# Kernel optimization log

Measured on AMD Instinct MI355X. Metric: run time of the kernel, lower is better.

## Reference

```python
import jax, jax.numpy as jnp
import numpy as np
import math

B, S, E, H, FF = 8, 1024, 1024, 16, 4096
HD = E // H
N_DOM = 1024          # boolean-domain size used in the custom scale
LN_EPS = 1e-5


def _layernorm(x, g, b, eps=LN_EPS):
    mu = jnp.mean(x, axis=-1, keepdims=True)
    var = jnp.var(x, axis=-1, keepdims=True)
    return (x - mu) * jax.lax.rsqrt(var + eps) * g + b


def setup_inputs() -> dict:
    key = jax.random.key(0)
    ks = jax.random.split(key, 8)
    s_e = 1.0 / math.sqrt(E)
    s_f = 1.0 / math.sqrt(FF)
    return {
        "x": jax.random.normal(ks[0], (B, S, E), jnp.float32),
        "in_proj_w": jax.random.normal(ks[1], (3 * E, E), jnp.float32) * s_e,
        "out_proj_w": jax.random.normal(ks[2], (E, E), jnp.float32) * s_e,
        "ln1_g": jnp.ones((E,), jnp.float32),
        "ln1_b": jnp.zeros((E,), jnp.float32),
        "ln2_g": jnp.ones((E,), jnp.float32),
        "ln2_b": jnp.zeros((E,), jnp.float32),
        "w1": jax.random.normal(ks[3], (FF, E), jnp.float32) * s_e,
        "b1": jax.random.normal(ks[4], (FF,), jnp.float32) * 0.01,
        "w2": jax.random.normal(ks[5], (E, FF), jnp.float32) * s_f,
        "b2": jax.random.normal(ks[6], (E,), jnp.float32) * 0.01,
    }


def reference(x, in_proj_w, out_proj_w, ln1_g, ln1_b, ln2_g, ln2_b, w1, b1, w2, b2):
    # --- custom multi-head attention (bias=False, dropout=0) ---
    qkv = jnp.einsum("bse,fe->bsf", x, in_proj_w)              # [B,S,3E]
    q, k, v = jnp.split(qkv, 3, axis=-1)
    q = q.reshape(B, S, H, HD)
    k = k.reshape(B, S, H, HD)
    v = v.reshape(B, S, H, HD)
    # nonstandard scale: sqrt(1/head_dim) * 2 * log(N)
    scale = math.sqrt(1.0 / HD) * 2.0 * math.log(N_DOM)
    scores = jnp.einsum("bqhd,bkhd->bhqk", q * scale, k)       # [B,H,S,S]
    attn = jax.nn.softmax(scores, axis=-1)
    ctx = jnp.einsum("bhqk,bkhd->bqhd", attn, v).reshape(B, S, E)
    attn_out = jnp.einsum("bse,fe->bsf", ctx, out_proj_w)      # [B,S,E]
    # --- residual + norm + FFN + residual + norm ---
    h = _layernorm(x + attn_out, ln1_g, ln1_b)
    ff = jnp.einsum("bsf,ef->bse", jax.nn.relu(jnp.einsum("bse,fe->bsf", h, w1) + b1), w2) + b2
    return _layernorm(h + ff, ln2_g, ln2_b)
```

## Files before the change

### kernel.cpp

```cpp
#include <hip/hip_runtime.h>
#include <cstdint>
#include <cmath>


typedef _Float16 f16;
typedef _Float16 f16x8 __attribute__((ext_vector_type(8)));
typedef _Float16 f16x4 __attribute__((ext_vector_type(4)));
typedef __bf16   bf16;
typedef __bf16   bf16x8 __attribute__((ext_vector_type(8)));
typedef __bf16   bf16x4 __attribute__((ext_vector_type(4)));
typedef float    f32x4  __attribute__((ext_vector_type(4)));

#define B_SZ  8
#define S_SZ  1024
#define E_SZ  1024
#define H_SZ  16
#define HD_SZ 64
#define FF_SZ 4096
#define MTOK  (B_SZ * S_SZ)

__device__ __forceinline__ void async_ld16(const void* g, void* l) {
  __builtin_amdgcn_global_load_lds(
      (const __attribute__((address_space(1))) void*)(uintptr_t)g,
      (__attribute__((address_space(3))) void*)(uint32_t)(uintptr_t)l,
      16, 0, 0);
}

__global__ void cast_kernel(const float* __restrict__ in, f16* __restrict__ out, int n4) {
  int i = blockIdx.x * blockDim.x + threadIdx.x;
  if (i < n4) {
    float4 f = ((const float4*)in)[i];
    f16x4 o = {(f16)f.x, (f16)f.y, (f16)f.z, (f16)f.w};
    ((f16x4*)out)[i] = o;
  }
}

template <bool OUT_F16, bool RELU>
__global__ void gemm_bt(const f16* __restrict__ A, const f16* __restrict__ Bm,
                        const float* __restrict__ bias, void* __restrict__ Cp,
                        int M, int N, int K, int bf16_from_bn) {
  __shared__ f16 As[128 * 64];
  __shared__ f16 Bs[128 * 64];

  const int tid  = threadIdx.x;
  const int wave = tid >> 6;
  const int lane = tid & 63;
  const int quad = lane >> 4;
  const int l16  = lane & 15;
  const int c7   = l16 & 7;
  const int wr   = wave >> 1;
  const int wc   = wave & 1;
  const int bm   = blockIdx.y;
  const int bn   = blockIdx.x;

  f32x4 acc[4][4];
#pragma unroll
  for (int i = 0; i < 4; i++)
#pragma unroll
    for (int j = 0; j < 4; j++) acc[i][j] = (f32x4){0.f, 0.f, 0.f, 0.f};

  const int rii  = wave * 8 + (lane >> 3);
  const int soct = (lane & 7) ^ (rii & 7);
  const f16* gA = A + ((size_t)bm * 128 + rii) * (size_t)K + soct * 8;
  const f16* gB = Bm + ((size_t)bn * 128 + rii) * (size_t)K + soct * 8;

  for (int k0 = 0; k0 < K; k0 += 64) {
    __syncthreads();
#pragma unroll
    for (int i = 0; i < 4; i++)
      async_ld16(gA + (size_t)i * 32 * K + k0, &As[(i * 32 + wave * 8) * 64]);
#pragma unroll
    for (int i = 0; i < 4; i++)
      async_ld16(gB + (size_t)i * 32 * K + k0, &Bs[(i * 32 + wave * 8) * 64]);
    __syncthreads();

#pragma unroll
    for (int kd2 = 0; kd2 < 2; kd2++) {
      f16x8 af[4], bfv[4];
#pragma unroll
      for (int mi = 0; mi < 4; mi++)
        af[mi] = *(const f16x8*)&As[(wr * 64 + mi * 16 + l16) * 64 + (((kd2 * 4 + quad) ^ c7) << 3)];
#pragma unroll
      for (int ni = 0; ni < 4; ni++)
        bfv[ni] = *(const f16x8*)&Bs[(wc * 64 + ni * 16 + l16) * 64 + (((kd2 * 4 + quad) ^ c7) << 3)];
#pragma unroll
      for (int mi = 0; mi < 4; mi++)
#pragma unroll
        for (int ni = 0; ni < 4; ni++)
          acc[mi][ni] = __builtin_amdgcn_mfma_f32_16x16x32_f16(af[mi], bfv[ni], acc[mi][ni], 0, 0, 0);
    }
  }

  const int rowBase = bm * 128 + wr * 64;
  const int colBase = bn * 128 + wc * 64;
  const bool store_bf16 = OUT_F16 && (bn >= bf16_from_bn);
#pragma unroll
  for (int ni = 0; ni < 4; ni++) {
    const int col = colBase + ni * 16 + l16;
    const float bv = (bias != nullptr) ? bias[col] : 0.f;
#pragma unroll
    for (int mi = 0; mi < 4; mi++) {
#pragma unroll
      for (int r = 0; r < 4; r++) {
        const int row = rowBase + mi * 16 + quad * 4 + r;
        float v = acc[mi][ni][r] + bv;
        if (RELU) v = fmaxf(v, 0.f);
        if (OUT_F16) {
          if (store_bf16)
            ((bf16*)Cp)[(size_t)row * N + col] = (bf16)v;
          else
            ((f16*)Cp)[(size_t)row * N + col] = (f16)v;
        } else {
          ((float*)Cp)[(size_t)row * N + col] = v;
        }
      }
    }
  }
}

__global__ __launch_bounds__(256, 3)
void attn_kernel(const f16* __restrict__ qkv, f16* __restrict__ ctx,
                 float scale2, float c2) {
  __shared__ __align__(16) char pool[49664];
  f16*  Qs = (f16*)pool;
  bf16* Ps = (bf16*)pool;
  bf16* Vt = (bf16*)(pool + 16384);
  f16*  Ks = (f16*)(pool + 33280);

  const int tid  = threadIdx.x;
  const int wave = tid >> 6;
  const int lane = tid & 63;
  const int quad = lane >> 4;
  const int l16  = lane & 15;
  const int c7   = l16 & 7;

  const int flat = blockIdx.x;
  const int bh   = flat & 127;
  const int qt   = flat >> 7;
  const int b    = bh >> 4;
  const int h    = bh & 15;

  const int rs = 3 * E_SZ;
  const size_t tokbase = (size_t)b * S_SZ;

  const int su  = lane >> 3;
  const int soc = (lane & 7) ^ su;

  {
    const f16* gq = qkv + (tokbase + qt * 128 + wave * 8 + su) * (size_t)rs + h * HD_SZ + soc * 8;
#pragma unroll
    for (int i = 0; i < 4; i++)
      async_ld16(gq + (size_t)i * 32 * rs, pool + (i * 32 + wave * 8) * 128);
  }
  __syncthreads();

  f16x8 aq[2][2];
#pragma unroll
  for (int mi = 0; mi < 2; mi++)
#pragma unroll
    for (int kd = 0; kd < 2; kd++) {
      const int row = wave * 32 + mi * 16 + l16;
      aq[mi][kd] = *(const f16x8*)&Qs[row * 64 + (((kd * 4 + quad) ^ c7) << 3)];
    }

  float Lpart[2] = {0.f, 0.f};
  f32x4 oacc[2][4];
#pragma unroll
  for (int mi = 0; mi < 2; mi++)
#pragma unroll
    for (int ni = 0; ni < 4; ni++) oacc[mi][ni] = (f32x4){0.f, 0.f, 0.f, 0.f};

  const int vc  = (tid & 7) * 8;
  const int vk0 = (tid >> 3) * 4;

  for (int t = 0; t < S_SZ / 128; t++) {
    __syncthreads();
    {
      const f16* gk = qkv + (tokbase + t * 128 + wave * 8 + su) * (size_t)rs + E_SZ + h * HD_SZ + soc * 8;
#pragma unroll
      for (int i = 0; i < 4; i++)
        async_ld16(gk + (size_t)i * 32 * rs, pool + 33280 + (i * 32 + wave * 8) * 128);
    }
    {
      const bf16* gv = (const bf16*)qkv + (tokbase + t * 128 + vk0) * (size_t)rs + 2 * E_SZ + h * HD_SZ + vc;
      bf16x8 v0 = *(const bf16x8*)(gv);
      bf16x8 v1 = *(const bf16x8*)(gv + rs);
      bf16x8 v2 = *(const bf16x8*)(gv + 2 * rs);
      bf16x8 v3 = *(const bf16x8*)(gv + 3 * rs);
#pragma unroll
      for (int e = 0; e < 8; e++) {
        bf16x4 pk = {v0[e], v1[e], v2[e], v3[e]};
        *(bf16x4*)&Vt[(vc + e) * 132 + vk0] = pk;
      }
    }
    __syncthreads();

    f32x4 sacc[2][8];
#pragma unroll
    for (int mi = 0; mi < 2; mi++)
#pragma unroll
      for (int nt = 0; nt < 8; nt++) sacc[mi][nt] = (f32x4){0.f, 0.f, 0.f, 0.f};
#pragma unroll
    for (int nt = 0; nt < 8; nt++) {
      const int krow = nt * 16 + l16;
#pragma unroll
      for (int kd = 0; kd < 2; kd++) {
        f16x8 bk = *(const f16x8*)&Ks[krow * 64 + (((kd * 4 + quad) ^ c7) << 3)];
#pragma unroll
        for (int mi = 0; mi < 2; mi++)
          sacc[mi][nt] = __builtin_amdgcn_mfma_f32_16x16x32_f16(bk, aq[mi][kd], sacc[mi][nt], 0, 0, 0);
      }
    }

#pragma unroll
    for (int mi = 0; mi < 2; mi++) {
#pragma unroll
      for (int nt = 0; nt < 8; nt++) {
#pragma unroll
        for (int r = 0; r < 4; r++) {
          float p = exp2f(fmaf(sacc[mi][nt][r], scale2, -c2));
          sacc[mi][nt][r] = p;
          Lpart[mi] += p;
        }
      }
    }

#pragma unroll
    for (int hf = 0; hf < 2; hf++) {
#pragma unroll
      for (int mi = 0; mi < 2; mi++) {
        const int prow = wave * 32 + mi * 16 + l16;
#pragma unroll
        for (int ntl = 0; ntl < 4; ntl++) {
          const f32x4 s4 = sacc[mi][hf * 4 + ntl];
          bf16x4 pk = {(bf16)s4[0], (bf16)s4[1], (bf16)s4[2], (bf16)s4[3]};
          const int oct = (2 * ntl + (quad >> 1)) ^ c7;
          *(bf16x4*)&Ps[prow * 64 + oct * 8 + (quad & 1) * 4] = pk;
        }
      }
#pragma unroll
      for (int kt = 0; kt < 2; kt++) {
        bf16x8 ap[2];
#pragma unroll
        for (int mi = 0; mi < 2; mi++) {
          const int prow = wave * 32 + mi * 16 + l16;
          ap[mi] = *(const bf16x8*)&Ps[prow * 64 + (((kt * 4 + quad) ^ c7) << 3)];
        }
#pragma unroll
        for (int ni = 0; ni < 4; ni++) {
          const int d = ni * 16 + l16;
          bf16x4 blo = *(const bf16x4*)&Vt[d * 132 + hf * 64 + kt * 32 + quad * 8];
          bf16x4 bhi = *(const bf16x4*)&Vt[d * 132 + hf * 64 + kt * 32 + quad * 8 + 4];
          bf16x8 bv = __builtin_shufflevector(blo, bhi, 0, 1, 2, 3, 4, 5, 6, 7);
#pragma unroll
          for (int mi = 0; mi < 2; mi++)
            oacc[mi][ni] = __builtin_amdgcn_mfma_f32_16x16x32_bf16(ap[mi], bv, oacc[mi][ni], 0, 0, 0);
        }
      }
    }
  }

#pragma unroll
  for (int mi = 0; mi < 2; mi++) {
    float Lfull = Lpart[mi];
    Lfull += __shfl_xor(Lfull, 16, 64);
    Lfull += __shfl_xor(Lfull, 32, 64);
#pragma unroll
    for (int r = 0; r < 4; r++) {
      const float Lr  = __shfl(Lfull, quad * 4 + r, 64);
      const float inv = 1.f / Lr;
      const int s = qt * 128 + wave * 32 + mi * 16 + quad * 4 + r;
#pragma unroll
      for (int ni = 0; ni < 4; ni++)
        ctx[(tokbase + s) * (size_t)E_SZ + h * HD_SZ + ni * 16 + l16] = (f16)(oacc[mi][ni][r] * inv);
    }
  }
}

__global__ void ln_kernel(const float* __restrict__ a, const float* __restrict__ res,
                          const float* __restrict__ g, const float* __restrict__ bta,
                          float* __restrict__ out32, f16* __restrict__ out16) {
  const int row  = blockIdx.x;
  const int tid  = threadIdx.x;
  const int wave = tid >> 6;
  const int lane = tid & 63;
  const size_t base = (size_t)row * 1024;
  const int c = tid * 4;

  float4 va = *(const float4*)&a[base + c];
  float4 vr = *(const float4*)&res[base + c];
  float v0 = va.x + vr.x, v1 = va.y + vr.y, v2 = va.z + vr.z, v3 = va.w + vr.w;

  __shared__ float r1[4], r2[4];
  float s = v0 + v1 + v2 + v3;
#pragma unroll
  for (int off = 32; off; off >>= 1) s += __shfl_xor(s, off, 64);
  if (lane == 0) r1[wave] = s;
  __syncthreads();
  const float mu = (r1[0] + r1[1] + r1[2] + r1[3]) * (1.f / 1024.f);

  float d0 = v0 - mu, d1 = v1 - mu, d2 = v2 - mu, d3 = v3 - mu;
  float ss = d0 * d0 + d1 * d1 + d2 * d2 + d3 * d3;
#pragma unroll
  for (int off = 32; off; off >>= 1) ss += __shfl_xor(ss, off, 64);
  if (lane == 0) r2[wave] = ss;
  __syncthreads();
  const float var = (r2[0] + r2[1] + r2[2] + r2[3]) * (1.f / 1024.f);
  const float rsq = rsqrtf(var + 1e-5f);

  float4 gg = *(const float4*)&g[c];
  float4 bb = *(const float4*)&bta[c];
  float o0 = d0 * rsq * gg.x + bb.x;
  float o1 = d1 * rsq * gg.y + bb.y;
  float o2 = d2 * rsq * gg.z + bb.z;
  float o3 = d3 * rsq * gg.w + bb.w;
  float4 o = {o0, o1, o2, o3};
  *(float4*)&out32[base + c] = o;
  if (out16 != nullptr) {
    f16x4 ob = {(f16)o0, (f16)o1, (f16)o2, (f16)o3};
    *(f16x4*)&out16[base + c] = ob;
  }
}

extern "C" void kernel_launch(void* const* d_in, const int* in_sizes, int n_in,
                              void* d_out, int out_size, void* d_ws, size_t ws_size,
                              hipStream_t stream) {
  const float* x    = (const float*)d_in[0];
  const float* wqkv = (const float*)d_in[1];
  const float* wo   = (const float*)d_in[2];
  const float* ln1g = (const float*)d_in[3];
  const float* ln1b = (const float*)d_in[4];
  const float* ln2g = (const float*)d_in[5];
  const float* ln2b = (const float*)d_in[6];
  const float* w1   = (const float*)d_in[7];
  const float* b1   = (const float*)d_in[8];
  const float* w2   = (const float*)d_in[9];
  const float* b2   = (const float*)d_in[10];
  float* out = (float*)d_out;

  char* ws = (char*)d_ws;
  f16* w_inb  = (f16*)(ws + 0);
  f16* w_outb = (f16*)(ws + 6291456);
  f16* w1b    = (f16*)(ws + 8388608);
  f16* w2b    = (f16*)(ws + 16777216);
  f16* xb     = (f16*)(ws + 25165824);
  f16* qkv    = (f16*)(ws + 41943040);
  f16* ctx    = (f16*)(ws + 92274688);
  f16* ff1    = (f16*)(ws + 41943040);
  float* tmp  = (float*)(ws + 109051904);
  float* hbuf = (float*)(ws + 142606336);
  f16* hb     = xb;

  const int NOBF = 1 << 30;

  cast_kernel<<<3072, 256, 0, stream>>>(wqkv, w_inb, 3 * E_SZ * E_SZ / 4);
  cast_kernel<<<1024, 256, 0, stream>>>(wo, w_outb, E_SZ * E_SZ / 4);
  cast_kernel<<<4096, 256, 0, stream>>>(w1, w1b, FF_SZ * E_SZ / 4);
  cast_kernel<<<4096, 256, 0, stream>>>(w2, w2b, E_SZ * FF_SZ / 4);
  cast_kernel<<<8192, 256, 0, stream>>>(x, xb, MTOK * E_SZ / 4);

  gemm_bt<true, false><<<dim3(3 * E_SZ / 128, MTOK / 128), 256, 0, stream>>>(
      xb, w_inb, nullptr, qkv, MTOK, 3 * E_SZ, E_SZ, 16);

  attn_kernel<<<1024, 256, 0, stream>>>(qkv, ctx, 2.5f, 60.0f);

  gemm_bt<false, false><<<dim3(E_SZ / 128, MTOK / 128), 256, 0, stream>>>(
      ctx, w_outb, nullptr, tmp, MTOK, E_SZ, E_SZ, NOBF);

  ln_kernel<<<MTOK, 256, 0, stream>>>(tmp, x, ln1g, ln1b, hbuf, hb);

  gemm_bt<true, true><<<dim3(FF_SZ / 128, MTOK / 128), 256, 0, stream>>>(
      hb, w1b, b1, ff1, MTOK, FF_SZ, E_SZ, NOBF);

  gemm_bt<false, false><<<dim3(E_SZ / 128, MTOK / 128), 256, 0, stream>>>(
      ff1, w2b, b2, tmp, MTOK, E_SZ, FF_SZ, NOBF);

  ln_kernel<<<MTOK, 256, 0, stream>>>(tmp, hbuf, ln2g, ln2b, out, nullptr);

  (void)in_sizes; (void)n_in; (void)out_size; (void)ws_size;
}
```

Baseline: 525.6 us.

## Use 32x32 MFMA in GEMMs, fuse residual adds, f16 intermediates, fold softmax scale

Switches the GEMM inner loop from 16x16x32 to 32x32x16 MFMA tiles. Residual additions move into the GEMM epilogues, and the intermediates become f16 instead of fp32, which removes an fp32 hidden buffer and shrinks LN traffic. The attention kernel pre-scales Q in f16 and starts the score accumulators at the softmax offset, dropping an FMA per score. The trade-off is lower precision: the residual stream is kept in f16, and the second residual uses the f16 LN1 output rather than fp32.

```diff
diff --git a/kernel.cpp b/kernel.cpp
--- a/kernel.cpp
+++ b/kernel.cpp
@@ -10,6 +10,7 @@
 typedef __bf16   bf16x8 __attribute__((ext_vector_type(8)));
 typedef __bf16   bf16x4 __attribute__((ext_vector_type(4)));
 typedef float    f32x4  __attribute__((ext_vector_type(4)));
+typedef float    f32x16 __attribute__((ext_vector_type(16)));
 
 #define B_SZ  8
 #define S_SZ  1024
@@ -35,12 +36,103 @@
   }
 }
 
-template <bool OUT_F16, bool RELU>
+template <bool RELU>
 __global__ void gemm_bt(const f16* __restrict__ A, const f16* __restrict__ Bm,
-                        const float* __restrict__ bias, void* __restrict__ Cp,
+                        const float* __restrict__ bias,
+                        const float* __restrict__ res32,
+                        const f16* __restrict__ res16,
+                        void* __restrict__ Cp,
                         int M, int N, int K, int bf16_from_bn) {
   __shared__ f16 As[128 * 64];
   __shared__ f16 Bs[128 * 64];
+
+  const int tid  = threadIdx.x;
+  const int wave = tid >> 6;
+  const int lane = tid & 63;
+  const int l32  = lane & 31;
+  const int hi   = lane >> 5;
+  const int wr   = wave >> 1;
+  const int wc   = wave & 1;
+  const int bm   = blockIdx.y;
+  const int bn   = blockIdx.x;
+
+  f32x16 acc[2][2];
+#pragma unroll
+  for (int i = 0; i < 2; i++)
+#pragma unroll
+    for (int j = 0; j < 2; j++)
+#pragma unroll
+      for (int e = 0; e < 16; e++) acc[i][j][e] = 0.f;
+
+  const int rii  = wave * 8 + (lane >> 3);
+  const int soct = (lane & 7) ^ (rii & 7);
+  const f16* gA = A + ((size_t)bm * 128 + rii) * (size_t)K + soct * 8;
+  const f16* gB = Bm + ((size_t)bn * 128 + rii) * (size_t)K + soct * 8;
+
+  for (int k0 = 0; k0 < K; k0 += 64) {
+    __syncthreads();
+#pragma unroll
+    for (int i = 0; i < 4; i++)
+      async_ld16(gA + (size_t)i * 32 * K + k0, &As[(i * 32 + wave * 8) * 64]);
+#pragma unroll
+    for (int i = 0; i < 4; i++)
+      async_ld16(gB + (size_t)i * 32 * K + k0, &Bs[(i * 32 + wave * 8) * 64]);
+    __syncthreads();
+
+#pragma unroll
+    for (int ph = 0; ph < 4; ph++) {
+      f16x8 af[2], bfv[2];
+#pragma unroll
+      for (int mi = 0; mi < 2; mi++) {
+        const int row = wr * 64 + mi * 32 + l32;
+        af[mi] = *(const f16x8*)&As[row * 64 + (((ph * 2 + hi) ^ (row & 7)) << 3)];
+      }
+#pragma unroll
+      for (int ni = 0; ni < 2; ni++) {
+        const int row = wc * 64 + ni * 32 + l32;
+        bfv[ni] = *(const f16x8*)&Bs[row * 64 + (((ph * 2 + hi) ^ (row & 7)) << 3)];
+      }
+#pragma unroll
+      for (int mi = 0; mi < 2; mi++)
+#pragma unroll
+        for (int ni = 0; ni < 2; ni++)
+          acc[mi][ni] = __builtin_amdgcn_mfma_f32_32x32x16_f16(af[mi], bfv[ni], acc[mi][ni], 0, 0, 0);
+    }
+  }
+
+  const int rowBase = bm * 128 + wr * 64;
+  const int colBase = bn * 128 + wc * 64;
+  const bool store_bf16 = (bn >= bf16_from_bn);
+#pragma unroll
+  for (int ni = 0; ni < 2; ni++) {
+    const int col = colBase + ni * 32 + l32;
+    const float bv = (bias != nullptr) ? bias[col] : 0.f;
+#pragma unroll
+    for (int mi = 0; mi < 2; mi++) {
+#pragma unroll
+      for (int reg = 0; reg < 16; reg++) {
+        const int row = rowBase + mi * 32 + (reg & 3) + 8 * (reg >> 2) + 4 * hi;
+        const size_t idx = (size_t)row * N + col;
+        float v = acc[mi][ni][reg] + bv;
+        if (res32 != nullptr) v += res32[idx];
+        else if (res16 != nullptr) v += (float)res16[idx];
+        if (RELU) v = fmaxf(v, 0.f);
+        if (store_bf16)
+          ((bf16*)Cp)[idx] = (bf16)v;
+        else
+          ((f16*)Cp)[idx] = (f16)v;
+      }
+    }
+  }
+}
+
+__global__ __launch_bounds__(256, 3)
+void attn_kernel(const f16* __restrict__ qkv, f16* __restrict__ ctx) {
+  __shared__ __align__(16) char pool[49664];
+  f16*  Qs = (f16*)pool;
+  bf16* Ps = (bf16*)pool;
+  bf16* Vt = (bf16*)(pool + 16384);
+  f16*  Ks = (f16*)(pool + 33280);
 
   const int tid  = threadIdx.x;
   const int wave = tid >> 6;
@@ -48,91 +140,6 @@
   const int quad = lane >> 4;
   const int l16  = lane & 15;
   const int c7   = l16 & 7;
-  const int wr   = wave >> 1;
-  const int wc   = wave & 1;
-  const int bm   = blockIdx.y;
-  const int bn   = blockIdx.x;
-
-  f32x4 acc[4][4];
-#pragma unroll
-  for (int i = 0; i < 4; i++)
-#pragma unroll
-    for (int j = 0; j < 4; j++) acc[i][j] = (f32x4){0.f, 0.f, 0.f, 0.f};
-
-  const int rii  = wave * 8 + (lane >> 3);
-  const int soct = (lane & 7) ^ (rii & 7);
-  const f16* gA = A + ((size_t)bm * 128 + rii) * (size_t)K + soct * 8;
-  const f16* gB = Bm + ((size_t)bn * 128 + rii) * (size_t)K + soct * 8;
-
-  for (int k0 = 0; k0 < K; k0 += 64) {
-    __syncthreads();
-#pragma unroll
-    for (int i = 0; i < 4; i++)
-      async_ld16(gA + (size_t)i * 32 * K + k0, &As[(i * 32 + wave * 8) * 64]);
-#pragma unroll
-    for (int i = 0; i < 4; i++)
-      async_ld16(gB + (size_t)i * 32 * K + k0, &Bs[(i * 32 + wave * 8) * 64]);
-    __syncthreads();
-
-#pragma unroll
-    for (int kd2 = 0; kd2 < 2; kd2++) {
-      f16x8 af[4], bfv[4];
-#pragma unroll
-      for (int mi = 0; mi < 4; mi++)
-        af[mi] = *(const f16x8*)&As[(wr * 64 + mi * 16 + l16) * 64 + (((kd2 * 4 + quad) ^ c7) << 3)];
-#pragma unroll
-      for (int ni = 0; ni < 4; ni++)
-        bfv[ni] = *(const f16x8*)&Bs[(wc * 64 + ni * 16 + l16) * 64 + (((kd2 * 4 + quad) ^ c7) << 3)];
-#pragma unroll
-      for (int mi = 0; mi < 4; mi++)
-#pragma unroll
-        for (int ni = 0; ni < 4; ni++)
-          acc[mi][ni] = __builtin_amdgcn_mfma_f32_16x16x32_f16(af[mi], bfv[ni], acc[mi][ni], 0, 0, 0);
-    }
-  }
-
-  const int rowBase = bm * 128 + wr * 64;
-  const int colBase = bn * 128 + wc * 64;
-  const bool store_bf16 = OUT_F16 && (bn >= bf16_from_bn);
-#pragma unroll
-  for (int ni = 0; ni < 4; ni++) {
-    const int col = colBase + ni * 16 + l16;
-    const float bv = (bias != nullptr) ? bias[col] : 0.f;
-#pragma unroll
-    for (int mi = 0; mi < 4; mi++) {
-#pragma unroll
-      for (int r = 0; r < 4; r++) {
-        const int row = rowBase + mi * 16 + quad * 4 + r;
-        float v = acc[mi][ni][r] + bv;
-        if (RELU) v = fmaxf(v, 0.f);
-        if (OUT_F16) {
-          if (store_bf16)
-            ((bf16*)Cp)[(size_t)row * N + col] = (bf16)v;
-          else
-            ((f16*)Cp)[(size_t)row * N + col] = (f16)v;
-        } else {
-          ((float*)Cp)[(size_t)row * N + col] = v;
-        }
-      }
-    }
-  }
-}
-
-__global__ __launch_bounds__(256, 3)
-void attn_kernel(const f16* __restrict__ qkv, f16* __restrict__ ctx,
-                 float scale2, float c2) {
-  __shared__ __align__(16) char pool[49664];
-  f16*  Qs = (f16*)pool;
-  bf16* Ps = (bf16*)pool;
-  bf16* Vt = (bf16*)(pool + 16384);
-  f16*  Ks = (f16*)(pool + 33280);
-
-  const int tid  = threadIdx.x;
-  const int wave = tid >> 6;
-  const int lane = tid & 63;
-  const int quad = lane >> 4;
-  const int l16  = lane & 15;
-  const int c7   = l16 & 7;
 
   const int flat = blockIdx.x;
   const int bh   = flat & 127;
@@ -161,6 +168,7 @@
     for (int kd = 0; kd < 2; kd++) {
       const int row = wave * 32 + mi * 16 + l16;
       aq[mi][kd] = *(const f16x8*)&Qs[row * 64 + (((kd * 4 + quad) ^ c7) << 3)];
+      aq[mi][kd] = aq[mi][kd] * (f16)2.5f;
     }
 
   float Lpart[2] = {0.f, 0.f};
@@ -199,7 +207,8 @@
 #pragma unroll
     for (int mi = 0; mi < 2; mi++)
 #pragma unroll
-      for (int nt = 0; nt < 8; nt++) sacc[mi][nt] = (f32x4){0.f, 0.f, 0.f, 0.f};
+      for (int nt = 0; nt < 8; nt++)
+        sacc[mi][nt] = (f32x4){-60.f, -60.f, -60.f, -60.f};
 #pragma unroll
     for (int nt = 0; nt < 8; nt++) {
       const int krow = nt * 16 + l16;
@@ -218,7 +227,7 @@
       for (int nt = 0; nt < 8; nt++) {
 #pragma unroll
         for (int r = 0; r < 4; r++) {
-          float p = exp2f(fmaf(sacc[mi][nt][r], scale2, -c2));
+          float p = exp2f(sacc[mi][nt][r]);
           sacc[mi][nt][r] = p;
           Lpart[mi] += p;
         }
@@ -277,7 +286,7 @@
   }
 }
 
-__global__ void ln_kernel(const float* __restrict__ a, const float* __restrict__ res,
+__global__ void ln_kernel(const f16* __restrict__ a,
                           const float* __restrict__ g, const float* __restrict__ bta,
                           float* __restrict__ out32, f16* __restrict__ out16) {
   const int row  = blockIdx.x;
@@ -287,9 +296,8 @@
   const size_t base = (size_t)row * 1024;
   const int c = tid * 4;
 
-  float4 va = *(const float4*)&a[base + c];
-  float4 vr = *(const float4*)&res[base + c];
-  float v0 = va.x + vr.x, v1 = va.y + vr.y, v2 = va.z + vr.z, v3 = va.w + vr.w;
+  f16x4 va = *(const f16x4*)&a[base + c];
+  float v0 = (float)va[0], v1 = (float)va[1], v2 = (float)va[2], v3 = (float)va[3];
 
   __shared__ float r1[4], r2[4];
   float s = v0 + v1 + v2 + v3;
@@ -314,8 +322,10 @@
   float o1 = d1 * rsq * gg.y + bb.y;
   float o2 = d2 * rsq * gg.z + bb.z;
   float o3 = d3 * rsq * gg.w + bb.w;
-  float4 o = {o0, o1, o2, o3};
-  *(float4*)&out32[base + c] = o;
+  if (out32 != nullptr) {
+    float4 o = {o0, o1, o2, o3};
+    *(float4*)&out32[base + c] = o;
+  }
   if (out16 != nullptr) {
     f16x4 ob = {(f16)o0, (f16)o1, (f16)o2, (f16)o3};
     *(f16x4*)&out16[base + c] = ob;
@@ -347,8 +357,7 @@
   f16* qkv    = (f16*)(ws + 41943040);
   f16* ctx    = (f16*)(ws + 92274688);
   f16* ff1    = (f16*)(ws + 41943040);
-  float* tmp  = (float*)(ws + 109051904);
-  float* hbuf = (float*)(ws + 142606336);
+  f16* tmp16  = (f16*)(ws + 109051904);
   f16* hb     = xb;
 
   const int NOBF = 1 << 30;
@@ -359,23 +368,23 @@
   cast_kernel<<<4096, 256, 0, stream>>>(w2, w2b, E_SZ * FF_SZ / 4);
   cast_kernel<<<8192, 256, 0, stream>>>(x, xb, MTOK * E_SZ / 4);
 
-  gemm_bt<true, false><<<dim3(3 * E_SZ / 128, MTOK / 128), 256, 0, stream>>>(
-      xb, w_inb, nullptr, qkv, MTOK, 3 * E_SZ, E_SZ, 16);
-
-  attn_kernel<<<1024, 256, 0, stream>>>(qkv, ctx, 2.5f, 60.0f);
-
-  gemm_bt<false, false><<<dim3(E_SZ / 128, MTOK / 128), 256, 0, stream>>>(
-      ctx, w_outb, nullptr, tmp, MTOK, E_SZ, E_SZ, NOBF);
-
-  ln_kernel<<<MTOK, 256, 0, stream>>>(tmp, x, ln1g, ln1b, hbuf, hb);
-
-  gemm_bt<true, true><<<dim3(FF_SZ / 128, MTOK / 128), 256, 0, stream>>>(
-      hb, w1b, b1, ff1, MTOK, FF_SZ, E_SZ, NOBF);
-
-  gemm_bt<false, false><<<dim3(E_SZ / 128, MTOK / 128), 256, 0, stream>>>(
-      ff1, w2b, b2, tmp, MTOK, E_SZ, FF_SZ, NOBF);
-
-  ln_kernel<<<MTOK, 256, 0, stream>>>(tmp, hbuf, ln2g, ln2b, out, nullptr);
+  gemm_bt<false><<<dim3(3 * E_SZ / 128, MTOK / 128), 256, 0, stream>>>(
+      xb, w_inb, nullptr, nullptr, nullptr, qkv, MTOK, 3 * E_SZ, E_SZ, 16);
+
+  attn_kernel<<<1024, 256, 0, stream>>>(qkv, ctx);
+
+  gemm_bt<false><<<dim3(E_SZ / 128, MTOK / 128), 256, 0, stream>>>(
+      ctx, w_outb, nullptr, x, nullptr, tmp16, MTOK, E_SZ, E_SZ, NOBF);
+
+  ln_kernel<<<MTOK, 256, 0, stream>>>(tmp16, ln1g, ln1b, nullptr, hb);
+
+  gemm_bt<true><<<dim3(FF_SZ / 128, MTOK / 128), 256, 0, stream>>>(
+      hb, w1b, b1, nullptr, nullptr, ff1, MTOK, FF_SZ, E_SZ, NOBF);
+
+  gemm_bt<false><<<dim3(E_SZ / 128, MTOK / 128), 256, 0, stream>>>(
+      ff1, w2b, b2, nullptr, hb, tmp16, MTOK, E_SZ, FF_SZ, NOBF);
+
+  ln_kernel<<<MTOK, 256, 0, stream>>>(tmp16, ln2g, ln2b, out, nullptr);
 
   (void)in_sizes; (void)n_in; (void)out_size; (void)ws_size;
 }
```

Result: slower. 578.8 us (+10.1%).
